# Performance work log

Measured on AMD Instinct MI355X. Metric: run time of the kernel, lower is better.

The kernel has to match this reference:

```python
import jax, jax.numpy as jnp
import numpy as np

NUM_HEADS = 8


def setup_inputs() -> dict:
    key = jax.random.key(0)
    N, D = 131072, 512
    ks = jax.random.split(key, 10)
    inv = 1.0 / np.sqrt(D)
    return {
        "unit_embeddings": jax.random.normal(ks[0], (N, D), dtype=jnp.float32),
        "mask": jnp.ones((N,), dtype=bool),
        "mil_query": jax.random.normal(ks[1], (D,), dtype=jnp.float32),
        "Wq": jax.random.uniform(ks[2], (D, D), jnp.float32, -inv, inv),
        "bq": jax.random.uniform(ks[3], (D,), jnp.float32, -inv, inv),
        "Wk": jax.random.uniform(ks[4], (D, D), jnp.float32, -inv, inv),
        "bk": jax.random.uniform(ks[5], (D,), jnp.float32, -inv, inv),
        "Wv": jax.random.uniform(ks[6], (D, D), jnp.float32, -inv, inv),
        "bv": jax.random.uniform(ks[7], (D,), jnp.float32, -inv, inv),
        "Wo": jax.random.uniform(ks[8], (D, D), jnp.float32, -inv, inv),
        "bo": jax.random.uniform(ks[9], (D,), jnp.float32, -inv, inv),
    }


def reference(unit_embeddings, mask, mil_query, Wq, bq, Wk, bk, Wv, bv, Wo, bo):
    N, D = unit_embeddings.shape
    H = NUM_HEADS
    hd = D // H
    scale = np.float32(np.sqrt(hd))
    # The torch module expands a single learned query to N copies and takes the
    # diagonal of the NxN per-head score matrix; mathematically scores[h,n] = q_h . k_h[n] / scale.
    q = mil_query @ Wq.T + bq                       # (D,)
    K = unit_embeddings @ Wk.T + bk                 # (N, D)
    V = unit_embeddings @ Wv.T + bv                 # (N, D)
    qh = q.reshape(H, hd)                           # (H, hd)
    Kh = K.reshape(N, H, hd)
    Vh = V.reshape(N, H, hd)
    scores = jnp.einsum('hd,nhd->hn', qh, Kh) / scale   # (H, N)
    scores = jnp.where(mask[None, :], scores, -jnp.inf)
    w = jax.nn.softmax(scores, axis=-1)             # (H, N); dropout is identity at eval
    weighted = jnp.einsum('hn,nhd->hd', w, Vh)      # (H, hd)
    # torch does .transpose(0,1).contiguous().view(D): flatten in (hd, H) order
    flat = weighted.T.reshape(D)
    package_embedding = flat @ Wo.T + bo            # (D,)
    final_attention_weights = w.mean(axis=0)        # (N,)
    return package_embedding, final_attention_weights
```

## Files before the change

### kernel.cpp

```cpp
#include <hip/hip_runtime.h>

#define NN 131072
#define DD 512
#define HH 8
#define NPART 512

__device__ __forceinline__ float wave_sum64(float x) {
  float t;
#define DPPADD(ctrl)                                                                     \
  t = __int_as_float(__builtin_amdgcn_update_dpp(0, __float_as_int(x), ctrl, 0xf, 0xf, true)); \
  x += t;
  DPPADD(0x111)
  DPPADD(0x112)
  DPPADD(0x114)
  DPPADD(0x118)
  DPPADD(0x142)
  DPPADD(0x143)
#undef DPPADD
  return x;
}

__device__ __forceinline__ float rdlane(float v, int l) {
  return __int_as_float(__builtin_amdgcn_readlane(__float_as_int(v), l));
}

__device__ __forceinline__ float dpp_xor1(float x) {
  return __int_as_float(__builtin_amdgcn_update_dpp(0, __float_as_int(x), 0xB1, 0xf, 0xf, true));
}
__device__ __forceinline__ float dpp_xor2(float x) {
  return __int_as_float(__builtin_amdgcn_update_dpp(0, __float_as_int(x), 0x4E, 0xf, 0xf, true));
}

__global__ __launch_bounds__(256) void kA_q(const float* __restrict__ Wq,
                                            const float* __restrict__ bq,
                                            const float* __restrict__ mq,
                                            float* __restrict__ q) {
  int lane = threadIdx.x & 63;
  int gw = blockIdx.x * 4 + (threadIdx.x >> 6);
  const float4* wr = (const float4*)(Wq + (size_t)gw * DD);
  const float4* m4 = (const float4*)mq;
  float4 w0 = wr[lane], w1 = wr[64 + lane];
  float4 m0 = m4[lane], m1 = m4[64 + lane];
  float p = w0.x * m0.x + w0.y * m0.y + w0.z * m0.z + w0.w * m0.w +
            w1.x * m1.x + w1.y * m1.y + w1.z * m1.z + w1.w * m1.w;
  p = wave_sum64(p);
  if (lane == 63) q[gw] = p + bq[gw];
}

__global__ __launch_bounds__(256) void kB_kq(const float* __restrict__ Wk,
                                             const float* __restrict__ bk,
                                             const float* __restrict__ q,
                                             float* __restrict__ kq,
                                             float* __restrict__ cq) {
  int T = blockIdx.x * 256 + threadIdx.x;
  int h = T >> 9, j = T & 511;
  float acc = 0.f;
#pragma unroll 8
  for (int d = 0; d < 64; ++d)
    acc += q[h * 64 + d] * Wk[(size_t)(h * 64 + d) * DD + j];
  kq[T] = acc;
  if (T < HH) {
    float c = 0.f;
    for (int d = 0; d < 64; ++d) c += q[T * 64 + d] * bk[T * 64 + d];
    cq[T] = c;
  }
}

__global__ __launch_bounds__(256, 2) void kFused(const float* __restrict__ emb,
                                                 const float* __restrict__ kqg,
                                                 const float* __restrict__ cqp,
                                                 float* __restrict__ scoresT,
                                                 float2* __restrict__ mz_part,
                                                 float* __restrict__ part) {
  __shared__ float lds[4 * 4096];

  const int lane = threadIdx.x & 63;
  const int wid = threadIdx.x >> 6;
  const int u = blockIdx.x;
  const int hbase = wid * 2;
  const size_t rowbase = (size_t)u * 256;

  float c[2][8];
#pragma unroll
  for (int hh = 0; hh < 2; ++hh) {
    int h = hbase + hh;
    float4 x = *(const float4*)(kqg + h * 512 + 4 * lane);
    float4 y = *(const float4*)(kqg + h * 512 + 256 + 4 * lane);
    c[hh][0] = x.x; c[hh][1] = x.y; c[hh][2] = x.z; c[hh][3] = x.w;
    c[hh][4] = y.x; c[hh][5] = y.y; c[hh][6] = y.z; c[hh][7] = y.w;
  }
  const float cq_v = cqp[hbase + (lane & 1)];
  asm volatile("s_waitcnt vmcnt(0)" ::: "memory");

  float acc[2][8];
#pragma unroll
  for (int hh = 0; hh < 2; ++hh)
#pragma unroll
    for (int k = 0; k < 8; ++k) acc[hh][k] = 0.f;
  float m_v = -3.0e38f;
  float z_v = 0.f;

#define STAGE(ch)                                                                        \
  do {                                                                                   \
    int slot_ = (ch) & 3;                                                                \
    const float* gsrc_ = emb + (rowbase + (size_t)(ch) * 8) * 512 + wid * 1024;          \
    float* ldst_ = &lds[slot_ * 4096 + wid * 1024];                                      \
    _Pragma("unroll")                                                                    \
    for (int i_ = 0; i_ < 4; ++i_) {                                                     \
      __builtin_amdgcn_global_load_lds(                                                  \
          (const __attribute__((address_space(1))) void*)(gsrc_ + i_ * 256 + lane * 4),  \
          (__attribute__((address_space(3))) void*)(ldst_ + i_ * 256), 16, 0, 0);        \
    }                                                                                    \
  } while (0)

  STAGE(0);
  STAGE(1);
  STAGE(2);

#pragma unroll 1
  for (int ch = 0; ch < 32; ++ch) {
    if (ch == 0 || ch == 31) {
      asm volatile("s_waitcnt vmcnt(8)" ::: "memory");
    } else if (ch == 1 || ch == 30) {
      asm volatile("s_waitcnt vmcnt(12)" ::: "memory");
    } else {
      asm volatile("s_waitcnt vmcnt(16)" ::: "memory");
    }
    __builtin_amdgcn_s_barrier();
    asm volatile("" ::: "memory");

    if (ch + 3 < 32) STAGE(ch + 3);

    const float* sl = &lds[(ch & 3) * 4096];
#pragma unroll
    for (int st = 0; st < 4; ++st) {
      float4 ea0 = *(const float4*)(sl + (st * 2 + 0) * 512 + 4 * lane);
      float4 eb0 = *(const float4*)(sl + (st * 2 + 0) * 512 + 256 + 4 * lane);
      float4 ea1 = *(const float4*)(sl + (st * 2 + 1) * 512 + 4 * lane);
      float4 eb1 = *(const float4*)(sl + (st * 2 + 1) * 512 + 256 + 4 * lane);

      float s0 = ea0.x * c[0][0] + ea0.y * c[0][1] + ea0.z * c[0][2] + ea0.w * c[0][3] +
                 eb0.x * c[0][4] + eb0.y * c[0][5] + eb0.z * c[0][6] + eb0.w * c[0][7];
      float s1 = ea0.x * c[1][0] + ea0.y * c[1][1] + ea0.z * c[1][2] + ea0.w * c[1][3] +
                 eb0.x * c[1][4] + eb0.y * c[1][5] + eb0.z * c[1][6] + eb0.w * c[1][7];
      float s2 = ea1.x * c[0][0] + ea1.y * c[0][1] + ea1.z * c[0][2] + ea1.w * c[0][3] +
                 eb1.x * c[0][4] + eb1.y * c[0][5] + eb1.z * c[0][6] + eb1.w * c[0][7];
      float s3 = ea1.x * c[1][0] + ea1.y * c[1][1] + ea1.z * c[1][2] + ea1.w * c[1][3] +
                 eb1.x * c[1][4] + eb1.y * c[1][5] + eb1.z * c[1][6] + eb1.w * c[1][7];

      float m0 = (lane & 1) ? s1 : s0, d0 = (lane & 1) ? s0 : s1;
      float m1 = (lane & 1) ? s3 : s2, d1 = (lane & 1) ? s2 : s3;
      float r0 = m0 + dpp_xor1(d0);
      float r1 = m1 + dpp_xor1(d1);
      float mm = (lane & 2) ? r1 : r0, dd = (lane & 2) ? r0 : r1;
      float v = mm + dpp_xor2(dd);
      v += __shfl_xor(v, 4, 64);
      v += __shfl_xor(v, 8, 64);
      v += __shfl_xor(v, 16, 64);
      v += __shfl_xor(v, 32, 64);
      v = (v + cq_v) * 0.125f;

      int row = ch * 8 + st * 2;
      if (lane < 4)
        scoresT[(rowbase + row + (lane >> 1)) * 8 + hbase + (lane & 1)] = v;

      float tmax = fmaxf(v, __shfl_xor(v, 2, 64));
      if (__any(tmax > m_v + 8.0f)) {
        float m_new = fmaxf(m_v, tmax);
        float f = __expf(m_v - m_new);
        z_v *= f;
        m_v = m_new;
        float f0 = rdlane(f, 0), f1 = rdlane(f, 1);
        acc[0][0] *= f0; acc[0][1] *= f0; acc[0][2] *= f0; acc[0][3] *= f0;
        acc[0][4] *= f0; acc[0][5] *= f0; acc[0][6] *= f0; acc[0][7] *= f0;
        acc[1][0] *= f1; acc[1][1] *= f1; acc[1][2] *= f1; acc[1][3] *= f1;
        acc[1][4] *= f1; acc[1][5] *= f1; acc[1][6] *= f1; acc[1][7] *= f1;
      }
      float w = __expf(v - m_v);
      z_v += w;
      float w00 = rdlane(w, 0), w01 = rdlane(w, 1);
      float w10 = rdlane(w, 2), w11 = rdlane(w, 3);
      acc[0][0] += w00 * ea0.x + w10 * ea1.x; acc[0][1] += w00 * ea0.y + w10 * ea1.y;
      acc[0][2] += w00 * ea0.z + w10 * ea1.z; acc[0][3] += w00 * ea0.w + w10 * ea1.w;
      acc[0][4] += w00 * eb0.x + w10 * eb1.x; acc[0][5] += w00 * eb0.y + w10 * eb1.y;
      acc[0][6] += w00 * eb0.z + w10 * eb1.z; acc[0][7] += w00 * eb0.w + w10 * eb1.w;
      acc[1][0] += w01 * ea0.x + w11 * ea1.x; acc[1][1] += w01 * ea0.y + w11 * ea1.y;
      acc[1][2] += w01 * ea0.z + w11 * ea1.z; acc[1][3] += w01 * ea0.w + w11 * ea1.w;
      acc[1][4] += w01 * eb0.x + w11 * eb1.x; acc[1][5] += w01 * eb0.y + w11 * eb1.y;
      acc[1][6] += w01 * eb0.z + w11 * eb1.z; acc[1][7] += w01 * eb0.w + w11 * eb1.w;
    }
  }
#undef STAGE

  float zc = z_v + __shfl_xor(z_v, 2, 64);
  if (lane < 2) mz_part[(size_t)u * 8 + hbase + lane] = make_float2(m_v, zc);

#pragma unroll
  for (int hh = 0; hh < 2; ++hh) {
    float4 v0 = make_float4(acc[hh][0], acc[hh][1], acc[hh][2], acc[hh][3]);
    float4 v1 = make_float4(acc[hh][4], acc[hh][5], acc[hh][6], acc[hh][7]);
    *(float4*)(part + (size_t)u * 4096 + (hbase + hh) * 512 + 4 * lane) = v0;
    *(float4*)(part + (size_t)u * 4096 + (hbase + hh) * 512 + 256 + 4 * lane) = v1;
  }
}

__device__ __forceinline__ float2 mz_combine(float2 A, float2 B) {
  float M = fmaxf(A.x, B.x);
  float Z = A.y * __expf(A.x - M) + B.y * __expf(B.x - M);
  return make_float2(M, Z);
}

__global__ __launch_bounds__(256) void kMZ(const float2* __restrict__ mzp,
                                           float2* __restrict__ mzf) {
  __shared__ float2 red[256];
  int t = threadIdx.x, h = blockIdx.x;
  float2 acc = make_float2(-3.0e38f, 0.f);
  for (int i = t; i < NPART; i += 256) acc = mz_combine(acc, mzp[(size_t)i * 8 + h]);
  red[t] = acc;
  __syncthreads();
  for (int off = 128; off >= 1; off >>= 1) {
    if (t < off) red[t] = mz_combine(red[t], red[t + off]);
    __syncthreads();
  }
  if (t == 0) mzf[h] = make_float2(red[0].x, 1.0f / red[0].y);
}

__global__ __launch_bounds__(256) void kC1(const float* __restrict__ part,
                                           const float2* __restrict__ mzp,
                                           const float2* __restrict__ mzf,
                                           float* __restrict__ part2) {
  __shared__ float f_lds[16];
  int t = threadIdx.x;
  int bc = blockIdx.x & 31, oc = blockIdx.x >> 5;
  int h = oc >> 1;
  float2 MZ = mzf[h];
  if (t < 16) {
    float2 mz = mzp[(size_t)(bc * 16 + t) * 8 + h];
    f_lds[t] = __expf(mz.x - MZ.x) * MZ.y;
  }
  __syncthreads();
  int idx = oc * 256 + t;
  float acc = 0.f;
#pragma unroll 4
  for (int j = 0; j < 16; ++j)
    acc += f_lds[j] * part[(size_t)(bc * 16 + j) * 4096 + idx];
  part2[(size_t)bc * 4096 + idx] = acc;
}

__global__ __launch_bounds__(256) void kC2(const float* __restrict__ part2,
                                           float* __restrict__ s_final) {
  int idx = blockIdx.x * 256 + threadIdx.x;
  float acc = 0.f;
#pragma unroll 8
  for (int bc = 0; bc < 32; ++bc) acc += part2[(size_t)bc * 4096 + idx];
  s_final[idx] = acc;
}

__global__ __launch_bounds__(256) void kFAW(const float* __restrict__ scoresT,
                                            const float2* __restrict__ mzf,
                                            float* __restrict__ faw) {
  int n = blockIdx.x * 256 + threadIdx.x;
  float4 s0 = *(const float4*)(scoresT + (size_t)n * 8);
  float4 s1 = *(const float4*)(scoresT + (size_t)n * 8 + 4);
  float sv[8] = {s0.x, s0.y, s0.z, s0.w, s1.x, s1.y, s1.z, s1.w};
  float sum = 0.f;
#pragma unroll
  for (int h = 0; h < 8; ++h) {
    float2 mz = mzf[h];
    sum += __expf(sv[h] - mz.x) * mz.y;
  }
  faw[n] = sum * 0.125f;
}

__global__ __launch_bounds__(256) void kP5a(const float* __restrict__ Wv,
                                            const float* __restrict__ bv,
                                            const float* __restrict__ s_final,
                                            float* __restrict__ flat) {
  int lane = threadIdx.x & 63;
  int r = blockIdx.x * 4 + (threadIdx.x >> 6);
  int h = r >> 6, i = r & 63;
  const float4* wr = (const float4*)(Wv + (size_t)r * 512);
  const float4* sh = (const float4*)(s_final + h * 512);
  float4 w0 = wr[lane], w1 = wr[64 + lane];
  float4 s0 = sh[lane], s1 = sh[64 + lane];
  float p = w0.x * s0.x + w0.y * s0.y + w0.z * s0.z + w0.w * s0.w +
            w1.x * s1.x + w1.y * s1.y + w1.z * s1.z + w1.w * s1.w;
  p = wave_sum64(p);
  if (lane == 63) flat[i * 8 + h] = p + bv[r];
}

__global__ __launch_bounds__(256) void kP5b(const float* __restrict__ Wo,
                                            const float* __restrict__ bo,
                                            const float* __restrict__ flat,
                                            float* __restrict__ out) {
  int lane = threadIdx.x & 63;
  int d = blockIdx.x * 4 + (threadIdx.x >> 6);
  const float4* wr = (const float4*)(Wo + (size_t)d * 512);
  const float4* fl = (const float4*)flat;
  float4 w0 = wr[lane], w1 = wr[64 + lane];
  float4 f0 = fl[lane], f1 = fl[64 + lane];
  float p = w0.x * f0.x + w0.y * f0.y + w0.z * f0.z + w0.w * f0.w +
            w1.x * f1.x + w1.y * f1.y + w1.z * f1.z + w1.w * f1.w;
  p = wave_sum64(p);
  if (lane == 63) out[d] = p + bo[d];
}

extern "C" void kernel_launch(void* const* d_in, const int* in_sizes, int n_in,
                              void* d_out, int out_size, void* d_ws, size_t ws_size,
                              hipStream_t stream) {
  const float* emb = (const float*)d_in[0];
  const float* mq = (const float*)d_in[2];
  const float* Wq = (const float*)d_in[3];
  const float* bq = (const float*)d_in[4];
  const float* Wk = (const float*)d_in[5];
  const float* bk = (const float*)d_in[6];
  const float* Wv = (const float*)d_in[7];
  const float* bv = (const float*)d_in[8];
  const float* Wo = (const float*)d_in[9];
  const float* bo = (const float*)d_in[10];
  float* out = (float*)d_out;
  float* ws = (float*)d_ws;

  float* q = ws + 0;
  float* kq = ws + 512;
  float* cq = ws + 4608;
  float2* mz_part = (float2*)(ws + 4624);
  float2* mz_final = (float2*)(ws + 12816);
  float* s_final = ws + 12832;
  float* flat = ws + 16928;
  float* scoresT = ws + 17440;
  float* part2 = ws + 1066016;
  float* part = ws + 1197088;

  hipLaunchKernelGGL(kA_q, dim3(128), dim3(256), 0, stream, Wq, bq, mq, q);
  hipLaunchKernelGGL(kB_kq, dim3(16), dim3(256), 0, stream, Wk, bk, q, kq, cq);
  hipLaunchKernelGGL(kFused, dim3(512), dim3(256), 0, stream, emb, kq, cq, scoresT,
                     mz_part, part);
  hipLaunchKernelGGL(kMZ, dim3(8), dim3(256), 0, stream, mz_part, mz_final);
  hipLaunchKernelGGL(kC1, dim3(512), dim3(256), 0, stream, part, mz_part, mz_final, part2);
  hipLaunchKernelGGL(kC2, dim3(16), dim3(256), 0, stream, part2, s_final);
  hipLaunchKernelGGL(kFAW, dim3(512), dim3(256), 0, stream, scoresT, mz_final, out + 512);
  hipLaunchKernelGGL(kP5a, dim3(128), dim3(256), 0, stream, Wv, bv, s_final, flat);
  hipLaunchKernelGGL(kP5b, dim3(128), dim3(256), 0, stream, Wo, bo, flat, out);
}
```

Measured before the change: 119.5 us.

## Replace LDS-staged pipeline with direct global loads and 4x more fused blocks

```diff
diff --git a/kernel.cpp b/kernel.cpp
--- a/kernel.cpp
+++ b/kernel.cpp
@@ -3,7 +3,7 @@
 #define NN 131072
 #define DD 512
 #define HH 8
-#define NPART 512
+#define NUNIT 2048
 
 __device__ __forceinline__ float wave_sum64(float x) {
   float t;
@@ -66,19 +66,16 @@
   }
 }
 
-__global__ __launch_bounds__(256, 2) void kFused(const float* __restrict__ emb,
+__global__ __launch_bounds__(256, 6) void kFused(const float* __restrict__ emb,
                                                  const float* __restrict__ kqg,
                                                  const float* __restrict__ cqp,
                                                  float* __restrict__ scoresT,
                                                  float2* __restrict__ mz_part,
                                                  float* __restrict__ part) {
-  __shared__ float lds[4 * 4096];
-
   const int lane = threadIdx.x & 63;
   const int wid = threadIdx.x >> 6;
   const int u = blockIdx.x;
   const int hbase = wid * 2;
-  const size_t rowbase = (size_t)u * 256;
 
   float c[2][8];
 #pragma unroll
@@ -90,7 +87,6 @@
     c[hh][4] = y.x; c[hh][5] = y.y; c[hh][6] = y.z; c[hh][7] = y.w;
   }
   const float cq_v = cqp[hbase + (lane & 1)];
-  asm volatile("s_waitcnt vmcnt(0)" ::: "memory");
 
   float acc[2][8];
 #pragma unroll
@@ -100,97 +96,65 @@
   float m_v = -3.0e38f;
   float z_v = 0.f;
 
-#define STAGE(ch)                                                                        \
-  do {                                                                                   \
-    int slot_ = (ch) & 3;                                                                \
-    const float* gsrc_ = emb + (rowbase + (size_t)(ch) * 8) * 512 + wid * 1024;          \
-    float* ldst_ = &lds[slot_ * 4096 + wid * 1024];                                      \
-    _Pragma("unroll")                                                                    \
-    for (int i_ = 0; i_ < 4; ++i_) {                                                     \
-      __builtin_amdgcn_global_load_lds(                                                  \
-          (const __attribute__((address_space(1))) void*)(gsrc_ + i_ * 256 + lane * 4),  \
-          (__attribute__((address_space(3))) void*)(ldst_ + i_ * 256), 16, 0, 0);        \
-    }                                                                                    \
-  } while (0)
-
-  STAGE(0);
-  STAGE(1);
-  STAGE(2);
+  const float4* e4 = (const float4*)emb + (size_t)u * 64 * 128;
 
 #pragma unroll 1
-  for (int ch = 0; ch < 32; ++ch) {
-    if (ch == 0 || ch == 31) {
-      asm volatile("s_waitcnt vmcnt(8)" ::: "memory");
-    } else if (ch == 1 || ch == 30) {
-      asm volatile("s_waitcnt vmcnt(12)" ::: "memory");
-    } else {
-      asm volatile("s_waitcnt vmcnt(16)" ::: "memory");
+  for (int tile = 0; tile < 32; ++tile) {
+    float4 ea0 = e4[(tile * 2 + 0) * 128 + lane];
+    float4 eb0 = e4[(tile * 2 + 0) * 128 + 64 + lane];
+    float4 ea1 = e4[(tile * 2 + 1) * 128 + lane];
+    float4 eb1 = e4[(tile * 2 + 1) * 128 + 64 + lane];
+
+    float s0 = ea0.x * c[0][0] + ea0.y * c[0][1] + ea0.z * c[0][2] + ea0.w * c[0][3] +
+               eb0.x * c[0][4] + eb0.y * c[0][5] + eb0.z * c[0][6] + eb0.w * c[0][7];
+    float s1 = ea0.x * c[1][0] + ea0.y * c[1][1] + ea0.z * c[1][2] + ea0.w * c[1][3] +
+               eb0.x * c[1][4] + eb0.y * c[1][5] + eb0.z * c[1][6] + eb0.w * c[1][7];
+    float s2 = ea1.x * c[0][0] + ea1.y * c[0][1] + ea1.z * c[0][2] + ea1.w * c[0][3] +
+               eb1.x * c[0][4] + eb1.y * c[0][5] + eb1.z * c[0][6] + eb1.w * c[0][7];
+    float s3 = ea1.x * c[1][0] + ea1.y * c[1][1] + ea1.z * c[1][2] + ea1.w * c[1][3] +
+               eb1.x * c[1][4] + eb1.y * c[1][5] + eb1.z * c[1][6] + eb1.w * c[1][7];
+
+    float m0 = (lane & 1) ? s1 : s0, d0 = (lane & 1) ? s0 : s1;
+    float m1 = (lane & 1) ? s3 : s2, d1 = (lane & 1) ? s2 : s3;
+    float r0 = m0 + dpp_xor1(d0);
+    float r1 = m1 + dpp_xor1(d1);
+    float mm = (lane & 2) ? r1 : r0, dd = (lane & 2) ? r0 : r1;
+    float v = mm + dpp_xor2(dd);
+    v += __shfl_xor(v, 4, 64);
+    v += __shfl_xor(v, 8, 64);
+    v += __shfl_xor(v, 16, 64);
+    v += __shfl_xor(v, 32, 64);
+    v = (v + cq_v) * 0.125f;
+
+    if (lane < 4)
+      scoresT[(size_t)(u * 64 + tile * 2 + (lane >> 1)) * 8 + hbase + (lane & 1)] = v;
+
+    float tmax = fmaxf(v, __shfl_xor(v, 2, 64));
+    if (__any(tmax > m_v + 8.0f)) {
+      float m_new = fmaxf(m_v, tmax);
+      float f = __expf(m_v - m_new);
+      z_v *= f;
+      m_v = m_new;
+      float f0 = rdlane(f, 0), f1 = rdlane(f, 1);
+      acc[0][0] *= f0; acc[0][1] *= f0; acc[0][2] *= f0; acc[0][3] *= f0;
+      acc[0][4] *= f0; acc[0][5] *= f0; acc[0][6] *= f0; acc[0][7] *= f0;
+      acc[1][0] *= f1; acc[1][1] *= f1; acc[1][2] *= f1; acc[1][3] *= f1;
+      acc[1][4] *= f1; acc[1][5] *= f1; acc[1][6] *= f1; acc[1][7] *= f1;
     }
-    __builtin_amdgcn_s_barrier();
-    asm volatile("" ::: "memory");
-
-    if (ch + 3 < 32) STAGE(ch + 3);
-
-    const float* sl = &lds[(ch & 3) * 4096];
-#pragma unroll
-    for (int st = 0; st < 4; ++st) {
-      float4 ea0 = *(const float4*)(sl + (st * 2 + 0) * 512 + 4 * lane);
-      float4 eb0 = *(const float4*)(sl + (st * 2 + 0) * 512 + 256 + 4 * lane);
-      float4 ea1 = *(const float4*)(sl + (st * 2 + 1) * 512 + 4 * lane);
-      float4 eb1 = *(const float4*)(sl + (st * 2 + 1) * 512 + 256 + 4 * lane);
-
-      float s0 = ea0.x * c[0][0] + ea0.y * c[0][1] + ea0.z * c[0][2] + ea0.w * c[0][3] +
-                 eb0.x * c[0][4] + eb0.y * c[0][5] + eb0.z * c[0][6] + eb0.w * c[0][7];
-      float s1 = ea0.x * c[1][0] + ea0.y * c[1][1] + ea0.z * c[1][2] + ea0.w * c[1][3] +
-                 eb0.x * c[1][4] + eb0.y * c[1][5] + eb0.z * c[1][6] + eb0.w * c[1][7];
-      float s2 = ea1.x * c[0][0] + ea1.y * c[0][1] + ea1.z * c[0][2] + ea1.w * c[0][3] +
-                 eb1.x * c[0][4] + eb1.y * c[0][5] + eb1.z * c[0][6] + eb1.w * c[0][7];
-      float s3 = ea1.x * c[1][0] + ea1.y * c[1][1] + ea1.z * c[1][2] + ea1.w * c[1][3] +
-                 eb1.x * c[1][4] + eb1.y * c[1][5] + eb1.z * c[1][6] + eb1.w * c[1][7];
-
-      float m0 = (lane & 1) ? s1 : s0, d0 = (lane & 1) ? s0 : s1;
-      float m1 = (lane & 1) ? s3 : s2, d1 = (lane & 1) ? s2 : s3;
-      float r0 = m0 + dpp_xor1(d0);
-      float r1 = m1 + dpp_xor1(d1);
-      float mm = (lane & 2) ? r1 : r0, dd = (lane & 2) ? r0 : r1;
-      float v = mm + dpp_xor2(dd);
-      v += __shfl_xor(v, 4, 64);
-      v += __shfl_xor(v, 8, 64);
-      v += __shfl_xor(v, 16, 64);
-      v += __shfl_xor(v, 32, 64);
-      v = (v + cq_v) * 0.125f;
-
-      int row = ch * 8 + st * 2;
-      if (lane < 4)
-        scoresT[(rowbase + row + (lane >> 1)) * 8 + hbase + (lane & 1)] = v;
-
-      float tmax = fmaxf(v, __shfl_xor(v, 2, 64));
-      if (__any(tmax > m_v + 8.0f)) {
-        float m_new = fmaxf(m_v, tmax);
-        float f = __expf(m_v - m_new);
-        z_v *= f;
-        m_v = m_new;
-        float f0 = rdlane(f, 0), f1 = rdlane(f, 1);
-        acc[0][0] *= f0; acc[0][1] *= f0; acc[0][2] *= f0; acc[0][3] *= f0;
-        acc[0][4] *= f0; acc[0][5] *= f0; acc[0][6] *= f0; acc[0][7] *= f0;
-        acc[1][0] *= f1; acc[1][1] *= f1; acc[1][2] *= f1; acc[1][3] *= f1;
-        acc[1][4] *= f1; acc[1][5] *= f1; acc[1][6] *= f1; acc[1][7] *= f1;
-      }
-      float w = __expf(v - m_v);
-      z_v += w;
-      float w00 = rdlane(w, 0), w01 = rdlane(w, 1);
-      float w10 = rdlane(w, 2), w11 = rdlane(w, 3);
-      acc[0][0] += w00 * ea0.x + w10 * ea1.x; acc[0][1] += w00 * ea0.y + w10 * ea1.y;
-      acc[0][2] += w00 * ea0.z + w10 * ea1.z; acc[0][3] += w00 * ea0.w + w10 * ea1.w;
-      acc[0][4] += w00 * eb0.x + w10 * eb1.x; acc[0][5] += w00 * eb0.y + w10 * eb1.y;
-      acc[0][6] += w00 * eb0.z + w10 * eb1.z; acc[0][7] += w00 * eb0.w + w10 * eb1.w;
-      acc[1][0] += w01 * ea0.x + w11 * ea1.x; acc[1][1] += w01 * ea0.y + w11 * ea1.y;
-      acc[1][2] += w01 * ea0.z + w11 * ea1.z; acc[1][3] += w01 * ea0.w + w11 * ea1.w;
-      acc[1][4] += w01 * eb0.x + w11 * eb1.x; acc[1][5] += w01 * eb0.y + w11 * eb1.y;
-      acc[1][6] += w01 * eb0.z + w11 * eb1.z; acc[1][7] += w01 * eb0.w + w11 * eb1.w;
-    }
-  }
-#undef STAGE
+    float w = __expf(v - m_v);
+    z_v += w;
+
+    float w00 = rdlane(w, 0), w01 = rdlane(w, 1);
+    float w10 = rdlane(w, 2), w11 = rdlane(w, 3);
+    acc[0][0] += w00 * ea0.x + w10 * ea1.x; acc[0][1] += w00 * ea0.y + w10 * ea1.y;
+    acc[0][2] += w00 * ea0.z + w10 * ea1.z; acc[0][3] += w00 * ea0.w + w10 * ea1.w;
+    acc[0][4] += w00 * eb0.x + w10 * eb1.x; acc[0][5] += w00 * eb0.y + w10 * eb1.y;
+    acc[0][6] += w00 * eb0.z + w10 * eb1.z; acc[0][7] += w00 * eb0.w + w10 * eb1.w;
+    acc[1][0] += w01 * ea0.x + w11 * ea1.x; acc[1][1] += w01 * ea0.y + w11 * ea1.y;
+    acc[1][2] += w01 * ea0.z + w11 * ea1.z; acc[1][3] += w01 * ea0.w + w11 * ea1.w;
+    acc[1][4] += w01 * eb0.x + w11 * eb1.x; acc[1][5] += w01 * eb0.y + w11 * eb1.y;
+    acc[1][6] += w01 * eb0.z + w11 * eb1.z; acc[1][7] += w01 * eb0.w + w11 * eb1.w;
+  }
 
   float zc = z_v + __shfl_xor(z_v, 2, 64);
   if (lane < 2) mz_part[(size_t)u * 8 + hbase + lane] = make_float2(m_v, zc);
@@ -215,7 +179,7 @@
   __shared__ float2 red[256];
   int t = threadIdx.x, h = blockIdx.x;
   float2 acc = make_float2(-3.0e38f, 0.f);
-  for (int i = t; i < NPART; i += 256) acc = mz_combine(acc, mzp[(size_t)i * 8 + h]);
+  for (int i = t; i < NUNIT; i += 256) acc = mz_combine(acc, mzp[(size_t)i * 8 + h]);
   red[t] = acc;
   __syncthreads();
   for (int off = 128; off >= 1; off >>= 1) {
@@ -229,21 +193,21 @@
                                            const float2* __restrict__ mzp,
                                            const float2* __restrict__ mzf,
                                            float* __restrict__ part2) {
-  __shared__ float f_lds[16];
+  __shared__ float f_lds[64];
   int t = threadIdx.x;
   int bc = blockIdx.x & 31, oc = blockIdx.x >> 5;
   int h = oc >> 1;
   float2 MZ = mzf[h];
-  if (t < 16) {
-    float2 mz = mzp[(size_t)(bc * 16 + t) * 8 + h];
+  if (t < 64) {
+    float2 mz = mzp[(size_t)(bc * 64 + t) * 8 + h];
     f_lds[t] = __expf(mz.x - MZ.x) * MZ.y;
   }
   __syncthreads();
   int idx = oc * 256 + t;
   float acc = 0.f;
 #pragma unroll 4
-  for (int j = 0; j < 16; ++j)
-    acc += f_lds[j] * part[(size_t)(bc * 16 + j) * 4096 + idx];
+  for (int j = 0; j < 64; ++j)
+    acc += f_lds[j] * part[(size_t)(bc * 64 + j) * 4096 + idx];
   part2[(size_t)bc * 4096 + idx] = acc;
 }
 
@@ -325,16 +289,16 @@
   float* kq = ws + 512;
   float* cq = ws + 4608;
   float2* mz_part = (float2*)(ws + 4624);
-  float2* mz_final = (float2*)(ws + 12816);
-  float* s_final = ws + 12832;
-  float* flat = ws + 16928;
-  float* scoresT = ws + 17440;
-  float* part2 = ws + 1066016;
-  float* part = ws + 1197088;
+  float2* mz_final = (float2*)(ws + 37392);
+  float* s_final = ws + 37408;
+  float* flat = ws + 41504;
+  float* scoresT = ws + 42016;
+  float* part2 = ws + 1090592;
+  float* part = ws + 1221664;
 
   hipLaunchKernelGGL(kA_q, dim3(128), dim3(256), 0, stream, Wq, bq, mq, q);
   hipLaunchKernelGGL(kB_kq, dim3(16), dim3(256), 0, stream, Wk, bk, q, kq, cq);
-  hipLaunchKernelGGL(kFused, dim3(512), dim3(256), 0, stream, emb, kq, cq, scoresT,
+  hipLaunchKernelGGL(kFused, dim3(2048), dim3(256), 0, stream, emb, kq, cq, scoresT,
                      mz_part, part);
   hipLaunchKernelGGL(kMZ, dim3(8), dim3(256), 0, stream, mz_part, mz_final);
   hipLaunchKernelGGL(kC1, dim3(512), dim3(256), 0, stream, part, mz_part, mz_final, part2);
```

Result: no change. 120.0 us (+0.4%).
